# Kernel tuning notes

Measured on AMD Instinct MI355X. Metric: run time of the kernel, lower is better.

## Reference

```python
import jax, jax.numpy as jnp
import numpy as np

N = 20000          # num nodes
C = 128            # in_channels
DEG = 32           # fixed neighborhood size (max nodes per group)
NUM_PIECES = 5
NEG = -99999.0     # padding value used before descending sort (as in original)


def setup_inputs() -> dict:
    key = jax.random.key(0)
    k1, k2, k3 = jax.random.split(key, 3)
    x = jax.random.normal(k1, (N, C), dtype=jnp.float32)
    # row sorted with uniform degree DEG (required by to_batch's cumsum indexing;
    # also makes max_degree static for jit)
    row = jnp.repeat(jnp.arange(N, dtype=jnp.int32), DEG)
    col = jax.random.randint(k2, (N * DEG,), 0, N, dtype=jnp.int32)
    edge_index = jnp.stack([row, col])                      # [2, E]
    weight = jax.random.normal(k3, (C, NUM_PIECES + 1), dtype=jnp.float32)
    return {"x": x, "edge_index": edge_index, "weight": weight}


def reference(x, edge_index, weight):
    row, col = edge_index[0], edge_index[1]
    E = row.shape[0]

    # --- to_batch: gather neighbor feats, scatter into padded dense batch ---
    gathered = x[col]                                                    # [E, C]
    num_nodes = jax.ops.segment_sum(jnp.ones((E,), jnp.int32), row,
                                    num_segments=N)                      # [N]
    cum = jnp.concatenate([jnp.zeros((1,), jnp.int32),
                           jnp.cumsum(num_nodes)])                       # [N+1]
    pos = jnp.arange(E, dtype=jnp.int32) - cum[row]                      # slot within group
    dense = jnp.zeros((N, DEG, C), x.dtype).at[row, pos].set(gathered)   # [N, DEG, C]
    dense = jnp.transpose(dense, (0, 2, 1))                              # [N, C, DEG]

    # --- fill_sizes: relative positions in [0,1] + validity mask ---
    n = num_nodes.astype(jnp.float32)                                    # [N]
    t = jnp.arange(DEG, dtype=jnp.float32)[None, :] / \
        jnp.clip(n - 1.0, 1.0)[:, None]                                  # [N, DEG]
    mask = (t <= 1.0)[:, None, :].astype(x.dtype)                        # [N, 1, DEG]
    sizes = jnp.minimum(t, 1.0)                                          # [N, DEG]

    # --- determine_weight: piecewise-linear interpolation of weight rows ---
    index = NUM_PIECES * sizes                                           # [N, DEG]
    idx = jnp.floor(index).astype(jnp.int32)
    frac = index - idx.astype(jnp.float32)
    left = weight.T[idx]                                                 # [N, DEG, C]
    right = weight.T[jnp.minimum(idx + 1, NUM_PIECES)]                   # [N, DEG, C]
    w = (1.0 - frac)[..., None] * left + frac[..., None] * right         # [N, DEG, C]
    w = jnp.transpose(w, (0, 2, 1))                                      # [N, C, DEG]

    # --- FSPool: push padding down, per-feature descending sort, weighted sum ---
    masked = dense + (1.0 - mask) * NEG                                  # [N, C, DEG]
    xs = -jnp.sort(-masked, axis=2)                                      # descending
    out = jnp.sum(xs * w * mask, axis=2)                                 # [N, C]
    return out
```

## Files before the change

### kernel.cpp

```cpp
#include <hip/hip_runtime.h>

#define C 128
#define DEG 32
#define NPIECES 5

typedef __fp16 h2 __attribute__((ext_vector_type(2)));

#define CD(P,i,j) { h2 _mx = __builtin_elementwise_max(P##i, P##j); \
                    P##j   = __builtin_elementwise_min(P##i, P##j); P##i = _mx; }
#define CA(P,i,j) { h2 _mn = __builtin_elementwise_min(P##i, P##j); \
                    P##j   = __builtin_elementwise_max(P##i, P##j); P##i = _mn; }

#define SORT_NET(P) \
 CD(P,0,1) CA(P,2,3) CD(P,4,5) CA(P,6,7) CD(P,8,9) CA(P,10,11) CD(P,12,13) CA(P,14,15) \
 CD(P,16,17) CA(P,18,19) CD(P,20,21) CA(P,22,23) CD(P,24,25) CA(P,26,27) CD(P,28,29) CA(P,30,31) \
 CD(P,0,2) CD(P,1,3) CA(P,4,6) CA(P,5,7) CD(P,8,10) CD(P,9,11) CA(P,12,14) CA(P,13,15) \
 CD(P,16,18) CD(P,17,19) CA(P,20,22) CA(P,21,23) CD(P,24,26) CD(P,25,27) CA(P,28,30) CA(P,29,31) \
 CD(P,0,1) CD(P,2,3) CA(P,4,5) CA(P,6,7) CD(P,8,9) CD(P,10,11) CA(P,12,13) CA(P,14,15) \
 CD(P,16,17) CD(P,18,19) CA(P,20,21) CA(P,22,23) CD(P,24,25) CD(P,26,27) CA(P,28,29) CA(P,30,31) \
 CD(P,0,4) CD(P,1,5) CD(P,2,6) CD(P,3,7) CA(P,8,12) CA(P,9,13) CA(P,10,14) CA(P,11,15) \
 CD(P,16,20) CD(P,17,21) CD(P,18,22) CD(P,19,23) CA(P,24,28) CA(P,25,29) CA(P,26,30) CA(P,27,31) \
 CD(P,0,2) CD(P,1,3) CD(P,4,6) CD(P,5,7) CA(P,8,10) CA(P,9,11) CA(P,12,14) CA(P,13,15) \
 CD(P,16,18) CD(P,17,19) CD(P,20,22) CD(P,21,23) CA(P,24,26) CA(P,25,27) CA(P,28,30) CA(P,29,31) \
 CD(P,0,1) CD(P,2,3) CD(P,4,5) CD(P,6,7) CA(P,8,9) CA(P,10,11) CA(P,12,13) CA(P,14,15) \
 CD(P,16,17) CD(P,18,19) CD(P,20,21) CD(P,22,23) CA(P,24,25) CA(P,26,27) CA(P,28,29) CA(P,30,31) \
 CD(P,0,8) CD(P,1,9) CD(P,2,10) CD(P,3,11) CD(P,4,12) CD(P,5,13) CD(P,6,14) CD(P,7,15) \
 CA(P,16,24) CA(P,17,25) CA(P,18,26) CA(P,19,27) CA(P,20,28) CA(P,21,29) CA(P,22,30) CA(P,23,31) \
 CD(P,0,4) CD(P,1,5) CD(P,2,6) CD(P,3,7) CD(P,8,12) CD(P,9,13) CD(P,10,14) CD(P,11,15) \
 CA(P,16,20) CA(P,17,21) CA(P,18,22) CA(P,19,23) CA(P,24,28) CA(P,25,29) CA(P,26,30) CA(P,27,31) \
 CD(P,0,2) CD(P,1,3) CD(P,4,6) CD(P,5,7) CD(P,8,10) CD(P,9,11) CD(P,12,14) CD(P,13,15) \
 CA(P,16,18) CA(P,17,19) CA(P,20,22) CA(P,21,23) CA(P,24,26) CA(P,25,27) CA(P,28,30) CA(P,29,31) \
 CD(P,0,1) CD(P,2,3) CD(P,4,5) CD(P,6,7) CD(P,8,9) CD(P,10,11) CD(P,12,13) CD(P,14,15) \
 CA(P,16,17) CA(P,18,19) CA(P,20,21) CA(P,22,23) CA(P,24,25) CA(P,26,27) CA(P,28,29) CA(P,30,31) \
 CD(P,0,16) CD(P,1,17) CD(P,2,18) CD(P,3,19) CD(P,4,20) CD(P,5,21) CD(P,6,22) CD(P,7,23) \
 CD(P,8,24) CD(P,9,25) CD(P,10,26) CD(P,11,27) CD(P,12,28) CD(P,13,29) CD(P,14,30) CD(P,15,31) \
 CD(P,0,8) CD(P,1,9) CD(P,2,10) CD(P,3,11) CD(P,4,12) CD(P,5,13) CD(P,6,14) CD(P,7,15) \
 CD(P,16,24) CD(P,17,25) CD(P,18,26) CD(P,19,27) CD(P,20,28) CD(P,21,29) CD(P,22,30) CD(P,23,31) \
 CD(P,0,4) CD(P,1,5) CD(P,2,6) CD(P,3,7) CD(P,8,12) CD(P,9,13) CD(P,10,14) CD(P,11,15) \
 CD(P,16,20) CD(P,17,21) CD(P,18,22) CD(P,19,23) CD(P,24,28) CD(P,25,29) CD(P,26,30) CD(P,27,31) \
 CD(P,0,2) CD(P,1,3) CD(P,4,6) CD(P,5,7) CD(P,8,10) CD(P,9,11) CD(P,12,14) CD(P,13,15) \
 CD(P,16,18) CD(P,17,19) CD(P,20,22) CD(P,21,23) CD(P,24,26) CD(P,25,27) CD(P,28,30) CD(P,29,31) \
 CD(P,0,1) CD(P,2,3) CD(P,4,5) CD(P,6,7) CD(P,8,9) CD(P,10,11) CD(P,12,13) CD(P,14,15) \
 CD(P,16,17) CD(P,18,19) CD(P,20,21) CD(P,22,23) CD(P,24,25) CD(P,26,27) CD(P,28,29) CD(P,30,31)

#define REP32(M,P) M(P,0) M(P,1) M(P,2) M(P,3) M(P,4) M(P,5) M(P,6) M(P,7) \
 M(P,8) M(P,9) M(P,10) M(P,11) M(P,12) M(P,13) M(P,14) M(P,15) \
 M(P,16) M(P,17) M(P,18) M(P,19) M(P,20) M(P,21) M(P,22) M(P,23) \
 M(P,24) M(P,25) M(P,26) M(P,27) M(P,28) M(P,29) M(P,30) M(P,31)

#define DECLV(P,i) h2 P##i;

#define PIN_ALL(P) \
    asm("" : "+v"(P##0),"+v"(P##1),"+v"(P##2),"+v"(P##3),"+v"(P##4),"+v"(P##5), \
             "+v"(P##6),"+v"(P##7),"+v"(P##8),"+v"(P##9),"+v"(P##10),"+v"(P##11), \
             "+v"(P##12),"+v"(P##13),"+v"(P##14),"+v"(P##15)); \
    asm("" : "+v"(P##16),"+v"(P##17),"+v"(P##18),"+v"(P##19),"+v"(P##20), \
             "+v"(P##21),"+v"(P##22),"+v"(P##23),"+v"(P##24),"+v"(P##25), \
             "+v"(P##26),"+v"(P##27),"+v"(P##28),"+v"(P##29),"+v"(P##30),"+v"(P##31));

#define GATH16(P,i) { \
    int _rb = rw[qpad + (i)]; \
    P##i = __builtin_bit_cast(h2, x16g[(unsigned)_rb + c2l]); }

#define GATH32(P,i) { \
    int _rb = rw[qpad + (i)]; \
    float2 _f = *(const float2*)(xg + (unsigned)_rb * 8 + 2 * c2l); \
    P##i = __builtin_amdgcn_cvt_pkrtz(_f.x, _f.y); }

#define ACCM(P,i) _acc += P##i * wh[i][c2l];

__global__ __launch_bounds__(256) void cvt_kernel(
    const float* __restrict__ x, unsigned* __restrict__ x16, int total4, int N)
{
    for (int i = blockIdx.x * 256 + threadIdx.x; i < total4; i += gridDim.x * 256) {
        float4 f = ((const float4*)x)[i];
        int node = i >> 5;
        int g = (i & 31) >> 3;
        uint2 u = make_uint2(
            __builtin_bit_cast(unsigned, __builtin_amdgcn_cvt_pkrtz(f.x, f.y)),
            __builtin_bit_cast(unsigned, __builtin_amdgcn_cvt_pkrtz(f.z, f.w)));
        ((uint2*)x16)[(size_t)(g * N + node) * 8 + (i & 7)] = u;
    }
}

template <bool F16>
__global__ __launch_bounds__(256, 6) void fspool_kernel(
    const float* __restrict__ x,
    const unsigned* __restrict__ x16,
    const int* __restrict__ col,
    const float* __restrict__ weight,
    float* __restrict__ out,
    int N, int wpg)
{
    const int g = blockIdx.x & 3;
    __shared__ h2 wh[DEG][16];
    __shared__ int rows[4][134];

    const int tid = threadIdx.x;
    for (int q = tid; q < DEG * 16; q += 256) {
        int j = q >> 4, cp = q & 15;
        int c0 = g * 32 + 2 * cp;
        float t = (float)j / 31.0f;
        float index = (float)NPIECES * fminf(t, 1.0f);
        float fidx = floorf(index);
        int idx = (int)fidx;
        float frac = index - fidx;
        int idx2 = (idx + 1 > NPIECES) ? NPIECES : (idx + 1);
        float w0 = (1.0f - frac) * weight[c0 * (NPIECES + 1) + idx]
                 + frac         * weight[c0 * (NPIECES + 1) + idx2];
        float w1 = (1.0f - frac) * weight[(c0 + 1) * (NPIECES + 1) + idx]
                 + frac         * weight[(c0 + 1) * (NPIECES + 1) + idx2];
        wh[j][cp] = __builtin_amdgcn_cvt_pkrtz(w0, w1);
    }
    __syncthreads();

    const int lane = tid & 63;
    const int wid  = tid >> 6;
    const int c2l  = lane & 15;
    const int q    = lane >> 4;
    const int qpad = q * 33;
    int* rw = rows[wid];
    const int wpad0 = (lane >> 5) * 33 + (lane & 31);

    const int wig = (blockIdx.x >> 2) * 4 + wid;
    const int nquads = (N + 3) >> 2;
    const unsigned* x16g = x16 + (size_t)g * N * 16;
    const float*    xg   = x + g * 32;

    int quad = wig;
    int cr0, cr1;
    if (quad < nquads) {
        int ce = quad * 128 + lane;
        cr0 = col[ce];
        cr1 = col[ce + 64];
    }

    for (; quad < nquads; quad += wpg) {
        rw[wpad0]      = cr0 * 16;
        rw[66 + wpad0] = cr1 * 16;

        int nq = quad + wpg;
        if (nq < nquads) {
            int ce = nq * 128 + lane;
            cr0 = col[ce];
            cr1 = col[ce + 64];
        }

        int node = quad * 4 + q;

        if constexpr (F16) {
            REP32(DECLV, v)
            REP32(GATH16, v)
            PIN_ALL(v)
            SORT_NET(v)
            h2 _acc; _acc[0] = (__fp16)0.f; _acc[1] = (__fp16)0.f;
            REP32(ACCM, v)
            if (node < N)
                *(float2*)(out + (size_t)node * C + g * 32 + 2 * c2l) =
                    make_float2((float)_acc[0], (float)_acc[1]);
        } else {
            REP32(DECLV, u)
            REP32(GATH32, u)
            PIN_ALL(u)
            SORT_NET(u)
            h2 _acc; _acc[0] = (__fp16)0.f; _acc[1] = (__fp16)0.f;
            REP32(ACCM, u)
            if (node < N)
                *(float2*)(out + (size_t)node * C + g * 32 + 2 * c2l) =
                    make_float2((float)_acc[0], (float)_acc[1]);
        }
    }
}

extern "C" void kernel_launch(void* const* d_in, const int* in_sizes, int n_in,
                              void* d_out, int out_size, void* d_ws, size_t ws_size,
                              hipStream_t stream) {
    const float* x      = (const float*)d_in[0];
    const int*   edge   = (const int*)d_in[1];
    const float* weight = (const float*)d_in[2];
    float*       out    = (float*)d_out;

    int N = in_sizes[0] / C;
    int E = in_sizes[1] / 2;
    const int* col = edge + E;

    const int grid = 2504;
    const int wpg  = grid;

    const size_t need = (size_t)N * (C / 2) * sizeof(unsigned);
    if (ws_size >= need) {
        unsigned* x16 = (unsigned*)d_ws;
        cvt_kernel<<<1024, 256, 0, stream>>>(x, x16, N * (C / 4), N);
        fspool_kernel<true><<<grid, 256, 0, stream>>>(x, x16, col, weight, out, N, wpg);
    } else {
        fspool_kernel<false><<<grid, 256, 0, stream>>>(x, nullptr, col, weight, out, N, wpg);
    }
}
```

Before: 42.34 us.

## Switch to odd-even merge sort network and hoist weights into registers

New measurement: 39.10 us. 1.08x faster.

```diff
diff --git a/kernel.cpp b/kernel.cpp
--- a/kernel.cpp
+++ b/kernel.cpp
@@ -6,68 +6,62 @@
 
 typedef __fp16 h2 __attribute__((ext_vector_type(2)));
 
-#define CD(P,i,j) { h2 _mx = __builtin_elementwise_max(P##i, P##j); \
-                    P##j   = __builtin_elementwise_min(P##i, P##j); P##i = _mx; }
-#define CA(P,i,j) { h2 _mn = __builtin_elementwise_min(P##i, P##j); \
-                    P##j   = __builtin_elementwise_max(P##i, P##j); P##i = _mn; }
+__device__ __forceinline__ void cas_desc(h2& a, h2& b) {
+    h2 mx = __builtin_elementwise_max(a, b);
+    b = __builtin_elementwise_min(a, b);
+    a = mx;
+}
+template<int I, int END, int R, int M>
+__device__ __forceinline__ void oe_merge_loop(h2* v) {
+    if constexpr (I + R < END) {
+        cas_desc(v[I], v[I + R]);
+        oe_merge_loop<I + M, END, R, M>(v);
+    }
+}
+template<int LO, int N, int R>
+__device__ __forceinline__ void oe_merge(h2* v) {
+    constexpr int M = R * 2;
+    if constexpr (M < N) {
+        oe_merge<LO, N, M>(v);
+        oe_merge<LO + R, N, M>(v);
+        oe_merge_loop<LO + R, LO + N, R, M>(v);
+    } else {
+        cas_desc(v[LO], v[LO + R]);
+    }
+}
+template<int LO, int N>
+__device__ __forceinline__ void oe_sort(h2* v) {
+    if constexpr (N > 1) {
+        constexpr int M = N / 2;
+        oe_sort<LO, M>(v);
+        oe_sort<LO + M, M>(v);
+        oe_merge<LO, N, 1>(v);
+    }
+}
 
-#define SORT_NET(P) \
- CD(P,0,1) CA(P,2,3) CD(P,4,5) CA(P,6,7) CD(P,8,9) CA(P,10,11) CD(P,12,13) CA(P,14,15) \
- CD(P,16,17) CA(P,18,19) CD(P,20,21) CA(P,22,23) CD(P,24,25) CA(P,26,27) CD(P,28,29) CA(P,30,31) \
- CD(P,0,2) CD(P,1,3) CA(P,4,6) CA(P,5,7) CD(P,8,10) CD(P,9,11) CA(P,12,14) CA(P,13,15) \
- CD(P,16,18) CD(P,17,19) CA(P,20,22) CA(P,21,23) CD(P,24,26) CD(P,25,27) CA(P,28,30) CA(P,29,31) \
- CD(P,0,1) CD(P,2,3) CA(P,4,5) CA(P,6,7) CD(P,8,9) CD(P,10,11) CA(P,12,13) CA(P,14,15) \
- CD(P,16,17) CD(P,18,19) CA(P,20,21) CA(P,22,23) CD(P,24,25) CD(P,26,27) CA(P,28,29) CA(P,30,31) \
- CD(P,0,4) CD(P,1,5) CD(P,2,6) CD(P,3,7) CA(P,8,12) CA(P,9,13) CA(P,10,14) CA(P,11,15) \
- CD(P,16,20) CD(P,17,21) CD(P,18,22) CD(P,19,23) CA(P,24,28) CA(P,25,29) CA(P,26,30) CA(P,27,31) \
- CD(P,0,2) CD(P,1,3) CD(P,4,6) CD(P,5,7) CA(P,8,10) CA(P,9,11) CA(P,12,14) CA(P,13,15) \
- CD(P,16,18) CD(P,17,19) CD(P,20,22) CD(P,21,23) CA(P,24,26) CA(P,25,27) CA(P,28,30) CA(P,29,31) \
- CD(P,0,1) CD(P,2,3) CD(P,4,5) CD(P,6,7) CA(P,8,9) CA(P,10,11) CA(P,12,13) CA(P,14,15) \
- CD(P,16,17) CD(P,18,19) CD(P,20,21) CD(P,22,23) CA(P,24,25) CA(P,26,27) CA(P,28,29) CA(P,30,31) \
- CD(P,0,8) CD(P,1,9) CD(P,2,10) CD(P,3,11) CD(P,4,12) CD(P,5,13) CD(P,6,14) CD(P,7,15) \
- CA(P,16,24) CA(P,17,25) CA(P,18,26) CA(P,19,27) CA(P,20,28) CA(P,21,29) CA(P,22,30) CA(P,23,31) \
- CD(P,0,4) CD(P,1,5) CD(P,2,6) CD(P,3,7) CD(P,8,12) CD(P,9,13) CD(P,10,14) CD(P,11,15) \
- CA(P,16,20) CA(P,17,21) CA(P,18,22) CA(P,19,23) CA(P,24,28) CA(P,25,29) CA(P,26,30) CA(P,27,31) \
- CD(P,0,2) CD(P,1,3) CD(P,4,6) CD(P,5,7) CD(P,8,10) CD(P,9,11) CD(P,12,14) CD(P,13,15) \
- CA(P,16,18) CA(P,17,19) CA(P,20,22) CA(P,21,23) CA(P,24,26) CA(P,25,27) CA(P,28,30) CA(P,29,31) \
- CD(P,0,1) CD(P,2,3) CD(P,4,5) CD(P,6,7) CD(P,8,9) CD(P,10,11) CD(P,12,13) CD(P,14,15) \
- CA(P,16,17) CA(P,18,19) CA(P,20,21) CA(P,22,23) CA(P,24,25) CA(P,26,27) CA(P,28,29) CA(P,30,31) \
- CD(P,0,16) CD(P,1,17) CD(P,2,18) CD(P,3,19) CD(P,4,20) CD(P,5,21) CD(P,6,22) CD(P,7,23) \
- CD(P,8,24) CD(P,9,25) CD(P,10,26) CD(P,11,27) CD(P,12,28) CD(P,13,29) CD(P,14,30) CD(P,15,31) \
- CD(P,0,8) CD(P,1,9) CD(P,2,10) CD(P,3,11) CD(P,4,12) CD(P,5,13) CD(P,6,14) CD(P,7,15) \
- CD(P,16,24) CD(P,17,25) CD(P,18,26) CD(P,19,27) CD(P,20,28) CD(P,21,29) CD(P,22,30) CD(P,23,31) \
- CD(P,0,4) CD(P,1,5) CD(P,2,6) CD(P,3,7) CD(P,8,12) CD(P,9,13) CD(P,10,14) CD(P,11,15) \
- CD(P,16,20) CD(P,17,21) CD(P,18,22) CD(P,19,23) CD(P,24,28) CD(P,25,29) CD(P,26,30) CD(P,27,31) \
- CD(P,0,2) CD(P,1,3) CD(P,4,6) CD(P,5,7) CD(P,8,10) CD(P,9,11) CD(P,12,14) CD(P,13,15) \
- CD(P,16,18) CD(P,17,19) CD(P,20,22) CD(P,21,23) CD(P,24,26) CD(P,25,27) CD(P,28,30) CD(P,29,31) \
- CD(P,0,1) CD(P,2,3) CD(P,4,5) CD(P,6,7) CD(P,8,9) CD(P,10,11) CD(P,12,13) CD(P,14,15) \
- CD(P,16,17) CD(P,18,19) CD(P,20,21) CD(P,22,23) CD(P,24,25) CD(P,26,27) CD(P,28,29) CD(P,30,31)
+#define REP32(M) M(0) M(1) M(2) M(3) M(4) M(5) M(6) M(7) M(8) M(9) M(10) M(11) \
+ M(12) M(13) M(14) M(15) M(16) M(17) M(18) M(19) M(20) M(21) M(22) M(23) \
+ M(24) M(25) M(26) M(27) M(28) M(29) M(30) M(31)
 
-#define REP32(M,P) M(P,0) M(P,1) M(P,2) M(P,3) M(P,4) M(P,5) M(P,6) M(P,7) \
- M(P,8) M(P,9) M(P,10) M(P,11) M(P,12) M(P,13) M(P,14) M(P,15) \
- M(P,16) M(P,17) M(P,18) M(P,19) M(P,20) M(P,21) M(P,22) M(P,23) \
- M(P,24) M(P,25) M(P,26) M(P,27) M(P,28) M(P,29) M(P,30) M(P,31)
+#define PIN_ALL \
+    asm("" : "+v"(v[0]),"+v"(v[1]),"+v"(v[2]),"+v"(v[3]),"+v"(v[4]),"+v"(v[5]), \
+             "+v"(v[6]),"+v"(v[7]),"+v"(v[8]),"+v"(v[9]),"+v"(v[10]),"+v"(v[11]), \
+             "+v"(v[12]),"+v"(v[13]),"+v"(v[14]),"+v"(v[15])); \
+    asm("" : "+v"(v[16]),"+v"(v[17]),"+v"(v[18]),"+v"(v[19]),"+v"(v[20]), \
+             "+v"(v[21]),"+v"(v[22]),"+v"(v[23]),"+v"(v[24]),"+v"(v[25]), \
+             "+v"(v[26]),"+v"(v[27]),"+v"(v[28]),"+v"(v[29]),"+v"(v[30]),"+v"(v[31]));
 
-#define DECLV(P,i) h2 P##i;
+#define GATH16(i) { \
+    int _rb = rw[qpad + (i)]; \
+    v[i] = __builtin_bit_cast(h2, x16g[(unsigned)_rb + c2l]); }
 
-#define PIN_ALL(P) \
-    asm("" : "+v"(P##0),"+v"(P##1),"+v"(P##2),"+v"(P##3),"+v"(P##4),"+v"(P##5), \
-             "+v"(P##6),"+v"(P##7),"+v"(P##8),"+v"(P##9),"+v"(P##10),"+v"(P##11), \
-             "+v"(P##12),"+v"(P##13),"+v"(P##14),"+v"(P##15)); \
-    asm("" : "+v"(P##16),"+v"(P##17),"+v"(P##18),"+v"(P##19),"+v"(P##20), \
-             "+v"(P##21),"+v"(P##22),"+v"(P##23),"+v"(P##24),"+v"(P##25), \
-             "+v"(P##26),"+v"(P##27),"+v"(P##28),"+v"(P##29),"+v"(P##30),"+v"(P##31));
-
-#define GATH16(P,i) { \
-    int _rb = rw[qpad + (i)]; \
-    P##i = __builtin_bit_cast(h2, x16g[(unsigned)_rb + c2l]); }
-
-#define GATH32(P,i) { \
+#define GATH32(i) { \
     int _rb = rw[qpad + (i)]; \
     float2 _f = *(const float2*)(xg + (unsigned)_rb * 8 + 2 * c2l); \
-    P##i = __builtin_amdgcn_cvt_pkrtz(_f.x, _f.y); }
+    v[i] = __builtin_amdgcn_cvt_pkrtz(_f.x, _f.y); }
 
-#define ACCM(P,i) _acc += P##i * wh[i][c2l];
+#define LDW(i)  const h2 W##i = wh[i][c2l];
+#define ACCM(i) _acc += v[i] * W##i;
 
 __global__ __launch_bounds__(256) void cvt_kernel(
     const float* __restrict__ x, unsigned* __restrict__ x16, int total4, int N)
@@ -84,7 +78,7 @@
 }
 
 template <bool F16>
-__global__ __launch_bounds__(256, 6) void fspool_kernel(
+__global__ __launch_bounds__(256, 4) void fspool_kernel(
     const float* __restrict__ x,
     const unsigned* __restrict__ x16,
     const int* __restrict__ col,
@@ -97,8 +91,8 @@
     __shared__ int rows[4][134];
 
     const int tid = threadIdx.x;
-    for (int q = tid; q < DEG * 16; q += 256) {
-        int j = q >> 4, cp = q & 15;
+    for (int p = tid; p < DEG * 16; p += 256) {
+        int j = p >> 4, cp = p & 15;
         int c0 = g * 32 + 2 * cp;
         float t = (float)j / 31.0f;
         float index = (float)NPIECES * fminf(t, 1.0f);
@@ -121,6 +115,8 @@
     const int qpad = q * 33;
     int* rw = rows[wid];
     const int wpad0 = (lane >> 5) * 33 + (lane & 31);
+
+    REP32(LDW)
 
     const int wig = (blockIdx.x >> 2) * 4 + wid;
     const int nquads = (N + 3) >> 2;
@@ -148,27 +144,19 @@
 
         int node = quad * 4 + q;
 
+        h2 v[32];
         if constexpr (F16) {
-            REP32(DECLV, v)
-            REP32(GATH16, v)
-            PIN_ALL(v)
-            SORT_NET(v)
-            h2 _acc; _acc[0] = (__fp16)0.f; _acc[1] = (__fp16)0.f;
-            REP32(ACCM, v)
-            if (node < N)
-                *(float2*)(out + (size_t)node * C + g * 32 + 2 * c2l) =
-                    make_float2((float)_acc[0], (float)_acc[1]);
+            REP32(GATH16)
         } else {
-            REP32(DECLV, u)
-            REP32(GATH32, u)
-            PIN_ALL(u)
-            SORT_NET(u)
-            h2 _acc; _acc[0] = (__fp16)0.f; _acc[1] = (__fp16)0.f;
-            REP32(ACCM, u)
-            if (node < N)
-                *(float2*)(out + (size_t)node * C + g * 32 + 2 * c2l) =
-                    make_float2((float)_acc[0], (float)_acc[1]);
+            REP32(GATH32)
         }
+        PIN_ALL
+        oe_sort<0, 32>(v);
+        h2 _acc; _acc[0] = (__fp16)0.f; _acc[1] = (__fp16)0.f;
+        REP32(ACCM)
+        if (node < N)
+            *(float2*)(out + (size_t)node * C + g * 32 + 2 * c2l) =
+                make_float2((float)_acc[0], (float)_acc[1]);
     }
 }
 
```
